# Performance work log

Hardware: AMD Instinct MI355X
Metric: run time of the kernel (lower is better)

The kernel has to match this reference:

```python
import jax, jax.numpy as jnp
import numpy as np

N_NODES = 50000
N_EDGES = 800000
IN_SIZE = 128
NUM_HEADS = 8
HEAD_DIM = IN_SIZE // NUM_HEADS  # qk/val head dim = 16


def setup_inputs() -> dict:
    key = jax.random.key(0)
    ks = jax.random.split(key, 16)
    d = IN_SIZE
    lim = 1.0 / np.sqrt(d)
    inp = {
        "in_feats": jax.random.normal(ks[0], (N_NODES, d), jnp.float32),
        "struc_feats": jax.random.normal(ks[1], (N_NODES, d), jnp.float32),
        "edge_weights": jax.random.uniform(ks[2], (N_EDGES,), jnp.float32),
        "ln_scale": jnp.ones((d,), jnp.float32),
        "ln_bias": jnp.zeros((d,), jnp.float32),
        "Ws": jax.random.uniform(ks[3], (d, d), jnp.float32, -lim, lim),
        "bs": jnp.zeros((d,), jnp.float32),
        "Wq": jax.random.uniform(ks[4], (d, d), jnp.float32, -lim, lim),
        "bq": jnp.zeros((d,), jnp.float32),
        "Wk": jax.random.uniform(ks[5], (d, d), jnp.float32, -lim, lim),
        "bk": jnp.zeros((d,), jnp.float32),
        "Wv": jax.random.uniform(ks[6], (d, d), jnp.float32, -lim, lim),
        "bv": jnp.zeros((d,), jnp.float32),
        "Wo": jax.random.uniform(ks[7], (d, d), jnp.float32, -lim, lim),
        "edge_ids": jax.random.randint(ks[8], (2, N_EDGES), 0, N_NODES, jnp.int64)
        if jax.config.jax_enable_x64 else jax.random.randint(ks[8], (2, N_EDGES), 0, N_NODES, jnp.int32),
    }
    return inp


def _layer_norm(x, scale, bias, eps=1e-5):
    mu = jnp.mean(x, axis=-1, keepdims=True)
    var = jnp.var(x, axis=-1, keepdims=True)
    return (x - mu) * jax.lax.rsqrt(var + eps) * scale + bias


def reference(in_feats, struc_feats, edge_weights, ln_scale, ln_bias,
              Ws, bs, Wq, bq, Wk, bk, Wv, bv, Wo, edge_ids):
    N = in_feats.shape[0]
    H, hd = NUM_HEADS, HEAD_DIM

    delta = _layer_norm(in_feats, ln_scale, ln_bias)           # pre-norm
    delta = jax.nn.gelu(delta, approximate=False)               # pre-activation (exact GELU, torch default)
    delta_struc = delta + struc_feats @ Ws.T + bs               # struc_proj add

    qry = (delta_struc @ Wq.T + bq) / np.sqrt(hd)                # [N, qk]
    keyf = delta_struc @ Wk.T + bk                               # [N, qk]
    val = delta @ Wv.T + bv                                      # [N, val]

    src, dst = edge_ids[0], edge_ids[1]                          # out[src] += A[src,dst] * val[dst]
    qe = qry[src].reshape(-1, H, hd)                             # [E, H, hd]
    ke = keyf[dst].reshape(-1, H, hd)                            # [E, H, hd]
    attn = jax.nn.sigmoid(jnp.sum(qe * ke, axis=-1))             # [E, H]
    attn = edge_weights[:, None] * attn

    msgs = attn[:, :, None] * val[dst].reshape(-1, H, hd)        # [E, H, hd]
    agg = jax.ops.segment_sum(msgs.reshape(-1, H * hd), src, num_segments=N)  # [N, val]

    out = agg @ Wo.T                                             # out_proj (no bias)
    return in_feats + out                                        # skip connection
```

## Files before the change

### kernel.cpp

```cpp
#include <hip/hip_runtime.h>
#include <math.h>

#define NF 128

typedef __attribute__((ext_vector_type(8))) short short8;
typedef __attribute__((ext_vector_type(4))) float floatx4;

__device__ __forceinline__ unsigned short f2bf(float f) {
    union { float x; unsigned int i; } c; c.x = f;
    unsigned int r = c.i + 0x7fffu + ((c.i >> 16) & 1u);
    return (unsigned short)(r >> 16);
}
__device__ __forceinline__ float bf2f(unsigned short u) {
    union { unsigned int i; float x; } c; c.i = ((unsigned int)u) << 16;
    return c.x;
}
__device__ __forceinline__ void unpack8(uint4 u, float* f) {
    union { unsigned int i; float x; } c;
    c.i = u.x << 16;          f[0] = c.x;
    c.i = u.x & 0xffff0000u;  f[1] = c.x;
    c.i = u.y << 16;          f[2] = c.x;
    c.i = u.y & 0xffff0000u;  f[3] = c.x;
    c.i = u.z << 16;          f[4] = c.x;
    c.i = u.z & 0xffff0000u;  f[5] = c.x;
    c.i = u.w << 16;          f[6] = c.x;
    c.i = u.w & 0xffff0000u;  f[7] = c.x;
}
__device__ __forceinline__ ushort4 pack4(float a, float b, float c, float d) {
    ushort4 h; h.x = f2bf(a); h.y = f2bf(b); h.z = f2bf(c); h.w = f2bf(d);
    return h;
}

__global__ __launch_bounds__(256) void wconv5_kernel(
    const float* __restrict__ a, const float* __restrict__ b,
    const float* __restrict__ c, const float* __restrict__ d,
    const float* __restrict__ e, unsigned short* __restrict__ o)
{
    int i = blockIdx.x * 256 + threadIdx.x;
    int w = i >> 14, j = i & 16383;
    const float* p = (w == 0) ? a : (w == 1) ? b : (w == 2) ? c : (w == 3) ? d : e;
    o[i] = f2bf(p[j]);
}


__device__ __forceinline__ void stage_w64(unsigned short (*Wh)[136],
                                          const unsigned short* Wg, int tid)
{
    const uint4* g = (const uint4*)Wg;
    #pragma unroll
    for (int p = 0; p < 4; ++p) {
        int idx = tid + p * 256;
        *(uint4*)&Wh[idx >> 4][(idx & 15) * 8] = g[idx];
    }
}

__device__ __forceinline__ void mfma4(const unsigned short (*A)[136],
                                      const unsigned short (*Wh)[136],
                                      int lg, int quad, int w, floatx4* acc4)
{
    #pragma unroll
    for (int ks = 0; ks < 4; ++ks) {
        short8 a = *(const short8*)&A[w * 16 + lg][ks * 32 + quad * 8];
        #pragma unroll
        for (int t = 0; t < 4; ++t) {
            short8 b = *(const short8*)&Wh[t * 16 + lg][ks * 32 + quad * 8];
            acc4[t] = __builtin_amdgcn_mfma_f32_16x16x32_bf16(a, b, acc4[t], 0, 0, 0);
        }
    }
}

__device__ __forceinline__ void emit_bf16(unsigned short (*Wst)[136],
                                          const floatx4* acc, const float* bias,
                                          float scale, unsigned short* outg,
                                          int m0, int M, int tid)
{
    int lane = tid & 63, w = tid >> 6, lg = lane & 15, quad = lane >> 4;
    __syncthreads();
    #pragma unroll
    for (int t = 0; t < 8; ++t) {
        int col = t * 16 + lg;
        float bvv = bias[col] * scale;
        #pragma unroll
        for (int r = 0; r < 4; ++r)
            Wst[w * 16 + quad * 4 + r][col] = f2bf(acc[t][r] * scale + bvv);
    }
    __syncthreads();
    #pragma unroll
    for (int p = 0; p < 4; ++p) {
        int idx = tid + p * 256;
        int row = idx >> 4, c16 = idx & 15;
        int gm = m0 + row;
        if (gm < M)
            *(uint4*)(outg + (size_t)gm * NF + c16 * 8) = *(const uint4*)&Wst[row][c16 * 8];
    }
    __syncthreads();
}

__global__ __launch_bounds__(256) void fused_node_kernel(
    const float* __restrict__ in_feats, const float* __restrict__ struc,
    const float* __restrict__ gamma, const float* __restrict__ beta,
    const unsigned short* __restrict__ Wall,
    const float* __restrict__ bs, const float* __restrict__ bq,
    const float* __restrict__ bk, const float* __restrict__ bv,
    unsigned short* __restrict__ qb, unsigned short* __restrict__ kb,
    unsigned short* __restrict__ vb, int M)
{
    __shared__ unsigned short Xd[64][136];
    __shared__ unsigned short Xs2[64][136];
    __shared__ unsigned short Wl[64][136];

    int tid = threadIdx.x;
    int m0 = blockIdx.x * 64;
    int lane = tid & 63, w = tid >> 6, lg = lane & 15, quad = lane >> 4;

    stage_w64(Wl, Wall, tid);
    {
        int row = tid >> 2, t4 = tid & 3;
        int gm = m0 + row;
        bool vr = gm < M;
        const float4* ip = (const float4*)(in_feats + (size_t)gm * NF) + t4 * 8;
        float4 xf[8];
        #pragma unroll
        for (int p = 0; p < 8; ++p)
            xf[p] = vr ? ip[p] : make_float4(0.f, 0.f, 0.f, 0.f);
        float s = 0.f, sq = 0.f;
        #pragma unroll
        for (int p = 0; p < 8; ++p) {
            s  += xf[p].x + xf[p].y + xf[p].z + xf[p].w;
            sq += xf[p].x * xf[p].x + xf[p].y * xf[p].y
                + xf[p].z * xf[p].z + xf[p].w * xf[p].w;
        }
        s  += __shfl_xor(s, 1, 64);  s  += __shfl_xor(s, 2, 64);
        sq += __shfl_xor(sq, 1, 64); sq += __shfl_xor(sq, 2, 64);
        float mu = s * (1.0f / 128.0f);
        float var = sq * (1.0f / 128.0f) - mu * mu;
        float rstd = rsqrtf(var + 1e-5f);
        const float4* gp = (const float4*)gamma + t4 * 8;
        const float4* bp = (const float4*)beta + t4 * 8;
        #pragma unroll
        for (int p = 0; p < 8; ++p) {
            float4 g4 = gp[p], b4 = bp[p];
            float o0 = (xf[p].x - mu) * rstd * g4.x + b4.x;
            float o1 = (xf[p].y - mu) * rstd * g4.y + b4.y;
            float o2 = (xf[p].z - mu) * rstd * g4.z + b4.z;
            float o3 = (xf[p].w - mu) * rstd * g4.w + b4.w;
            o0 = 0.5f * o0 * (1.0f + erff(o0 * 0.70710678118654752f));
            o1 = 0.5f * o1 * (1.0f + erff(o1 * 0.70710678118654752f));
            o2 = 0.5f * o2 * (1.0f + erff(o2 * 0.70710678118654752f));
            o3 = 0.5f * o3 * (1.0f + erff(o3 * 0.70710678118654752f));
            *(ushort4*)&Xd[row][t4 * 32 + p * 4] = pack4(o0, o1, o2, o3);
        }
        const float4* sp = (const float4*)(struc + (size_t)gm * NF) + t4 * 8;
        #pragma unroll
        for (int p = 0; p < 8; ++p) {
            float4 f = vr ? sp[p] : make_float4(0.f, 0.f, 0.f, 0.f);
            *(ushort4*)&Xs2[row][t4 * 32 + p * 4] = pack4(f.x, f.y, f.z, f.w);
        }
    }
    __syncthreads();

    floatx4 acc[8];
    #pragma unroll
    for (int t = 0; t < 8; ++t) acc[t] = (floatx4){0.f, 0.f, 0.f, 0.f};

    mfma4(Xs2, Wl, lg, quad, w, acc);
    __syncthreads();
    stage_w64(Wl, Wall + 8192, tid);
    __syncthreads();
    mfma4(Xs2, Wl, lg, quad, w, acc + 4);
    __syncthreads();

    #pragma unroll
    for (int t = 0; t < 8; ++t) {
        int col = t * 16 + lg;
        float bvv = bs[col];
        #pragma unroll
        for (int r = 0; r < 4; ++r) {
            int rl = w * 16 + quad * 4 + r;
            Xs2[rl][col] = f2bf(acc[t][r] + bvv + bf2f(Xd[rl][col]));
        }
    }
    stage_w64(Wl, Wall + 16384, tid);
    __syncthreads();

    #pragma unroll
    for (int t = 0; t < 8; ++t) acc[t] = (floatx4){0.f, 0.f, 0.f, 0.f};
    mfma4(Xs2, Wl, lg, quad, w, acc);
    __syncthreads();
    stage_w64(Wl, Wall + 16384 + 8192, tid);
    __syncthreads();
    mfma4(Xs2, Wl, lg, quad, w, acc + 4);
    emit_bf16(Wl, acc, bq, 0.25f, qb, m0, M, tid);

    stage_w64(Wl, Wall + 2 * 16384, tid);
    __syncthreads();
    #pragma unroll
    for (int t = 0; t < 8; ++t) acc[t] = (floatx4){0.f, 0.f, 0.f, 0.f};
    mfma4(Xs2, Wl, lg, quad, w, acc);
    __syncthreads();
    stage_w64(Wl, Wall + 2 * 16384 + 8192, tid);
    __syncthreads();
    mfma4(Xs2, Wl, lg, quad, w, acc + 4);
    emit_bf16(Wl, acc, bk, 1.0f, kb, m0, M, tid);

    stage_w64(Wl, Wall + 3 * 16384, tid);
    __syncthreads();
    #pragma unroll
    for (int t = 0; t < 8; ++t) acc[t] = (floatx4){0.f, 0.f, 0.f, 0.f};
    mfma4(Xd, Wl, lg, quad, w, acc);
    __syncthreads();
    stage_w64(Wl, Wall + 3 * 16384 + 8192, tid);
    __syncthreads();
    mfma4(Xd, Wl, lg, quad, w, acc + 4);
    emit_bf16(Wl, acc, bv, 1.0f, vb, m0, M, tid);
}

__global__ __launch_bounds__(256) void gemm_out_kernel(
    const unsigned short* __restrict__ Xb, const unsigned short* __restrict__ Wb,
    const float* __restrict__ addf, float* __restrict__ Y, int M)
{
    __shared__ unsigned short Xs[64][136];
    __shared__ unsigned short Wl[128][136];
    int tid = threadIdx.x;
    int m0 = blockIdx.x * 64;

    {
        const uint4* Wg = (const uint4*)Wb;
        #pragma unroll
        for (int p = 0; p < 8; ++p) {
            int idx = tid + p * 256;
            *(uint4*)&Wl[idx >> 4][(idx & 15) * 8] = Wg[idx];
        }
    }
    {
        const uint4* X = (const uint4*)Xb;
        #pragma unroll
        for (int p = 0; p < 4; ++p) {
            int idx = tid + p * 256;
            int row = idx >> 4, c16 = idx & 15;
            int gm = m0 + row;
            uint4 u = make_uint4(0u, 0u, 0u, 0u);
            if (gm < M) u = X[(size_t)gm * 16 + c16];
            *(uint4*)&Xs[row][c16 * 8] = u;
        }
    }
    __syncthreads();

    int lane = tid & 63, w = tid >> 6, lg = lane & 15, quad = lane >> 4;
    floatx4 acc[8];
    #pragma unroll
    for (int t = 0; t < 8; ++t) acc[t] = (floatx4){0.f, 0.f, 0.f, 0.f};
    #pragma unroll
    for (int ks = 0; ks < 4; ++ks) {
        short8 a = *(const short8*)&Xs[w * 16 + lg][ks * 32 + quad * 8];
        #pragma unroll
        for (int t = 0; t < 8; ++t) {
            short8 b = *(const short8*)&Wl[t * 16 + lg][ks * 32 + quad * 8];
            acc[t] = __builtin_amdgcn_mfma_f32_16x16x32_bf16(a, b, acc[t], 0, 0, 0);
        }
    }
    #pragma unroll
    for (int t = 0; t < 8; ++t) {
        int col = t * 16 + lg;
        #pragma unroll
        for (int r = 0; r < 4; ++r) {
            int gm = m0 + w * 16 + quad * 4 + r;
            if (gm >= M) continue;
            size_t off = (size_t)gm * NF + col;
            Y[off] = acc[t][r] + addf[off];
        }
    }
}

__global__ void hist_kernel(const int* __restrict__ eid, int* __restrict__ cnt, int E)
{
    int i = blockIdx.x * blockDim.x + threadIdx.x;
    if (i < E) atomicAdd(&cnt[eid[i]], 1);
}

__global__ __launch_bounds__(256) void scan1_kernel(
    const int* __restrict__ cnt, int* __restrict__ bsum, int n)
{
    int base = blockIdx.x * 1024;
    int s = 0;
    #pragma unroll
    for (int p = 0; p < 4; ++p) {
        int i = base + (int)threadIdx.x + p * 256;
        if (i < n) s += cnt[i];
    }
    #pragma unroll
    for (int m = 1; m <= 32; m <<= 1) s += __shfl_xor(s, m, 64);
    __shared__ int ws_[4];
    int wid = threadIdx.x >> 6;
    if ((threadIdx.x & 63) == 0) ws_[wid] = s;
    __syncthreads();
    if (threadIdx.x == 0) bsum[blockIdx.x] = ws_[0] + ws_[1] + ws_[2] + ws_[3];
}

__global__ __launch_bounds__(64) void scan2_kernel(
    int* __restrict__ bsum, int* __restrict__ row_start, int nb, int n)
{
    int lane = threadIdx.x;
    int v = (lane < nb) ? bsum[lane] : 0;
    int s = v;
    #pragma unroll
    for (int off = 1; off < 64; off <<= 1) {
        int t = __shfl_up(s, off, 64);
        if (lane >= off) s += t;
    }
    if (lane < nb) bsum[lane] = s - v;
    if (lane == 63) row_start[n] = s;
}

__global__ __launch_bounds__(256) void scan3_kernel(
    const int* __restrict__ cnt, const int* __restrict__ bsum,
    int* __restrict__ row_start, int* __restrict__ cursor, int n)
{
    int base = blockIdx.x * 1024;
    int tid = threadIdx.x, lane = tid & 63, wid = tid >> 6;
    int v[4]; int s = 0;
    #pragma unroll
    for (int p = 0; p < 4; ++p) {
        int i = base + tid * 4 + p;
        v[p] = (i < n) ? cnt[i] : 0;
        s += v[p];
    }
    int ss = s;
    #pragma unroll
    for (int off = 1; off < 64; off <<= 1) {
        int t = __shfl_up(ss, off, 64);
        if (lane >= off) ss += t;
    }
    __shared__ int wsum[4];
    if (lane == 63) wsum[wid] = ss;
    __syncthreads();
    int woff = 0;
    for (int j = 0; j < wid; ++j) woff += wsum[j];
    int a = bsum[blockIdx.x] + woff + (ss - s);
    #pragma unroll
    for (int p = 0; p < 4; ++p) {
        int i = base + tid * 4 + p;
        if (i < n) { row_start[i] = a; cursor[i] = a; a += v[p]; }
    }
}

__global__ void scatter_kernel(const int* __restrict__ eid, const float* __restrict__ ew,
                               int* __restrict__ cursor, int2* __restrict__ edata, int E)
{
    int i = blockIdx.x * blockDim.x + threadIdx.x;
    if (i < E) {
        int src = eid[i];
        int dst = eid[E + i];
        int pos = atomicAdd(&cursor[src], 1);
        edata[pos] = make_int2(dst, __float_as_int(ew[i]));
    }
}

__global__ __launch_bounds__(64) void aggregate_kernel(
    const unsigned short* __restrict__ Q, const unsigned short* __restrict__ Kf,
    const unsigned short* __restrict__ V, const int* __restrict__ row_start,
    const int2* __restrict__ edata, unsigned short* __restrict__ agg, int N)
{
    int node = blockIdx.x;
    int lane = threadIdx.x;
    int sg = lane >> 4, lg = lane & 15;
    int rs = row_start[node], re = row_start[node + 1];

    float qv[8];
    unpack8(*(const uint4*)(Q + (size_t)node * NF + lg * 8), qv);
    float acc[8];
    #pragma unroll
    for (int j = 0; j < 8; ++j) acc[j] = 0.f;

    int e = rs + sg;
    int2 ed = (e < re) ? edata[e] : make_int2(0, 0);
    for (int e0 = rs; e0 < re; e0 += 4) {
        int dst = ed.x;
        float wgt = __int_as_float(ed.y);
        int en = e0 + 4 + sg;
        int2 nxt = (en < re) ? edata[en] : make_int2(0, 0);

        float kv[8];
        unpack8(*(const uint4*)(Kf + (size_t)dst * NF + lg * 8), kv);
        float s = qv[0] * kv[0];
        #pragma unroll
        for (int j = 1; j < 8; ++j) s = fmaf(qv[j], kv[j], s);
        s += __shfl_xor(s, 1, 64);
        float a = wgt / (1.f + __expf(-s));

        float vv[8];
        unpack8(*(const uint4*)(V + (size_t)dst * NF + lg * 8), vv);
        #pragma unroll
        for (int j = 0; j < 8; ++j) acc[j] = fmaf(a, vv[j], acc[j]);
        ed = nxt;
    }
    #pragma unroll
    for (int j = 0; j < 8; ++j) {
        acc[j] += __shfl_xor(acc[j], 16, 64);
        acc[j] += __shfl_xor(acc[j], 32, 64);
    }
    if (sg == 0) {
        unsigned short* o = agg + (size_t)node * NF + lg * 8;
        *(ushort4*)o       = pack4(acc[0], acc[1], acc[2], acc[3]);
        *(ushort4*)(o + 4) = pack4(acc[4], acc[5], acc[6], acc[7]);
    }
}

extern "C" void kernel_launch(void* const* d_in, const int* in_sizes, int n_in,
                              void* d_out, int out_size, void* d_ws, size_t ws_size,
                              hipStream_t stream)
{
    const float* in_feats = (const float*)d_in[0];
    const float* struc    = (const float*)d_in[1];
    const float* eweights = (const float*)d_in[2];
    const float* ln_scale = (const float*)d_in[3];
    const float* ln_bias  = (const float*)d_in[4];
    const float* Ws       = (const float*)d_in[5];
    const float* bs       = (const float*)d_in[6];
    const float* Wq       = (const float*)d_in[7];
    const float* bq       = (const float*)d_in[8];
    const float* Wk       = (const float*)d_in[9];
    const float* bk       = (const float*)d_in[10];
    const float* Wv       = (const float*)d_in[11];
    const float* bv       = (const float*)d_in[12];
    const float* Wo       = (const float*)d_in[13];
    const int*   edge_ids = (const int*)d_in[14];
    float* out = (float*)d_out;

    int N = in_sizes[0] / NF;
    int E = in_sizes[2];

    size_t F = (size_t)N * NF;
    unsigned short* qb   = (unsigned short*)d_ws;
    unsigned short* kb   = qb + F;
    unsigned short* vb   = kb + F;
    unsigned short* aggb = vb + F;
    unsigned short* Wall = aggb + F;
    int2*  edata     = (int2*)(Wall + 5 * 16384);
    int*   cnt       = (int*)(edata + E);
    int*   row_start = cnt + N;
    int*   cursor    = row_start + N + 1;
    int*   bsum      = cursor + N;

    int gb  = (N + 63) / 64;
    int geb = (E + 255) / 256;
    int nb  = (N + 1023) / 1024;

    wconv5_kernel<<<(5 * 16384) / 256, 256, 0, stream>>>(Ws, Wq, Wk, Wv, Wo, Wall);

    hipMemsetAsync(cnt, 0, (size_t)N * sizeof(int), stream);
    hist_kernel<<<geb, 256, 0, stream>>>(edge_ids, cnt, E);
    scan1_kernel<<<nb, 256, 0, stream>>>(cnt, bsum, N);
    scan2_kernel<<<1, 64, 0, stream>>>(bsum, row_start, nb, N);
    scan3_kernel<<<nb, 256, 0, stream>>>(cnt, bsum, row_start, cursor, N);
    scatter_kernel<<<geb, 256, 0, stream>>>(edge_ids, eweights, cursor, edata, E);

    fused_node_kernel<<<gb, 256, 0, stream>>>(in_feats, struc, ln_scale, ln_bias,
                                              Wall, bs, bq, bk, bv, qb, kb, vb, N);

    aggregate_kernel<<<N, 64, 0, stream>>>(qb, kb, vb, row_start, edata, aggb, N);

    gemm_out_kernel<<<gb, 256, 0, stream>>>(aggb, Wall + 4 * 16384, in_feats, out, N);
}
```

Measured before the change: 328.5 us.

## Split fused node kernel, merge scan passes, batch aggregate nodes and unroll edges

The fused node kernel is split in two. One kernel computes delta and delta_struc and writes both to bf16 buffers, and a second kernel runs a 3-way grid over Q, K and V, each block holding the full weight in LDS. This trades extra global round-trips for more parallelism and fewer barriers. The scan2 kernel is removed: each scan3 block now sums the block totals itself. The aggregate kernel packs 4 nodes per 256-thread block and processes two edges per iteration to raise memory-level parallelism.

```diff
diff --git a/kernel.cpp b/kernel.cpp
--- a/kernel.cpp
+++ b/kernel.cpp
@@ -42,68 +42,11 @@
     o[i] = f2bf(p[j]);
 }
 
-
-__device__ __forceinline__ void stage_w64(unsigned short (*Wh)[136],
-                                          const unsigned short* Wg, int tid)
-{
-    const uint4* g = (const uint4*)Wg;
-    #pragma unroll
-    for (int p = 0; p < 4; ++p) {
-        int idx = tid + p * 256;
-        *(uint4*)&Wh[idx >> 4][(idx & 15) * 8] = g[idx];
-    }
-}
-
-__device__ __forceinline__ void mfma4(const unsigned short (*A)[136],
-                                      const unsigned short (*Wh)[136],
-                                      int lg, int quad, int w, floatx4* acc4)
-{
-    #pragma unroll
-    for (int ks = 0; ks < 4; ++ks) {
-        short8 a = *(const short8*)&A[w * 16 + lg][ks * 32 + quad * 8];
-        #pragma unroll
-        for (int t = 0; t < 4; ++t) {
-            short8 b = *(const short8*)&Wh[t * 16 + lg][ks * 32 + quad * 8];
-            acc4[t] = __builtin_amdgcn_mfma_f32_16x16x32_bf16(a, b, acc4[t], 0, 0, 0);
-        }
-    }
-}
-
-__device__ __forceinline__ void emit_bf16(unsigned short (*Wst)[136],
-                                          const floatx4* acc, const float* bias,
-                                          float scale, unsigned short* outg,
-                                          int m0, int M, int tid)
-{
-    int lane = tid & 63, w = tid >> 6, lg = lane & 15, quad = lane >> 4;
-    __syncthreads();
-    #pragma unroll
-    for (int t = 0; t < 8; ++t) {
-        int col = t * 16 + lg;
-        float bvv = bias[col] * scale;
-        #pragma unroll
-        for (int r = 0; r < 4; ++r)
-            Wst[w * 16 + quad * 4 + r][col] = f2bf(acc[t][r] * scale + bvv);
-    }
-    __syncthreads();
-    #pragma unroll
-    for (int p = 0; p < 4; ++p) {
-        int idx = tid + p * 256;
-        int row = idx >> 4, c16 = idx & 15;
-        int gm = m0 + row;
-        if (gm < M)
-            *(uint4*)(outg + (size_t)gm * NF + c16 * 8) = *(const uint4*)&Wst[row][c16 * 8];
-    }
-    __syncthreads();
-}
-
-__global__ __launch_bounds__(256) void fused_node_kernel(
+__global__ __launch_bounds__(256) void node_a_kernel(
     const float* __restrict__ in_feats, const float* __restrict__ struc,
     const float* __restrict__ gamma, const float* __restrict__ beta,
-    const unsigned short* __restrict__ Wall,
-    const float* __restrict__ bs, const float* __restrict__ bq,
-    const float* __restrict__ bk, const float* __restrict__ bv,
-    unsigned short* __restrict__ qb, unsigned short* __restrict__ kb,
-    unsigned short* __restrict__ vb, int M)
+    const unsigned short* __restrict__ Wsb, const float* __restrict__ bs,
+    unsigned short* __restrict__ deltab, unsigned short* __restrict__ dstrb, int M)
 {
     __shared__ unsigned short Xd[64][136];
     __shared__ unsigned short Xs2[64][136];
@@ -113,7 +56,14 @@
     int m0 = blockIdx.x * 64;
     int lane = tid & 63, w = tid >> 6, lg = lane & 15, quad = lane >> 4;
 
-    stage_w64(Wl, Wall, tid);
+    {
+        const uint4* g = (const uint4*)Wsb;
+        #pragma unroll
+        for (int p = 0; p < 4; ++p) {
+            int idx = tid + p * 256;
+            *(uint4*)&Wl[idx >> 4][(idx & 15) * 8] = g[idx];
+        }
+    }
     {
         int row = tid >> 2, t4 = tid & 3;
         int gm = m0 + row;
@@ -163,12 +113,34 @@
     #pragma unroll
     for (int t = 0; t < 8; ++t) acc[t] = (floatx4){0.f, 0.f, 0.f, 0.f};
 
-    mfma4(Xs2, Wl, lg, quad, w, acc);
-    __syncthreads();
-    stage_w64(Wl, Wall + 8192, tid);
-    __syncthreads();
-    mfma4(Xs2, Wl, lg, quad, w, acc + 4);
-    __syncthreads();
+    #pragma unroll
+    for (int ks = 0; ks < 4; ++ks) {
+        short8 a = *(const short8*)&Xs2[w * 16 + lg][ks * 32 + quad * 8];
+        #pragma unroll
+        for (int t = 0; t < 4; ++t) {
+            short8 b = *(const short8*)&Wl[t * 16 + lg][ks * 32 + quad * 8];
+            acc[t] = __builtin_amdgcn_mfma_f32_16x16x32_bf16(a, b, acc[t], 0, 0, 0);
+        }
+    }
+    __syncthreads();
+    {
+        const uint4* g = (const uint4*)(Wsb + 8192);
+        #pragma unroll
+        for (int p = 0; p < 4; ++p) {
+            int idx = tid + p * 256;
+            *(uint4*)&Wl[idx >> 4][(idx & 15) * 8] = g[idx];
+        }
+    }
+    __syncthreads();
+    #pragma unroll
+    for (int ks = 0; ks < 4; ++ks) {
+        short8 a = *(const short8*)&Xs2[w * 16 + lg][ks * 32 + quad * 8];
+        #pragma unroll
+        for (int t = 0; t < 4; ++t) {
+            short8 b = *(const short8*)&Wl[t * 16 + lg][ks * 32 + quad * 8];
+            acc[4 + t] = __builtin_amdgcn_mfma_f32_16x16x32_bf16(a, b, acc[4 + t], 0, 0, 0);
+        }
+    }
 
     #pragma unroll
     for (int t = 0; t < 8; ++t) {
@@ -180,39 +152,90 @@
             Xs2[rl][col] = f2bf(acc[t][r] + bvv + bf2f(Xd[rl][col]));
         }
     }
-    stage_w64(Wl, Wall + 16384, tid);
-    __syncthreads();
-
+    #pragma unroll
+    for (int p = 0; p < 4; ++p) {
+        int idx = lane + p * 64;
+        int row = w * 16 + (idx >> 4), c16 = idx & 15;
+        int gm = m0 + row;
+        if (gm < M) {
+            *(uint4*)(deltab + (size_t)gm * NF + c16 * 8) = *(const uint4*)&Xd[row][c16 * 8];
+            *(uint4*)(dstrb  + (size_t)gm * NF + c16 * 8) = *(const uint4*)&Xs2[row][c16 * 8];
+        }
+    }
+}
+
+__global__ __launch_bounds__(256) void node_qkv_kernel(
+    const unsigned short* __restrict__ deltab, const unsigned short* __restrict__ dstrb,
+    const unsigned short* __restrict__ Wall, const float* __restrict__ bq,
+    const float* __restrict__ bk, const float* __restrict__ bv,
+    unsigned short* __restrict__ qb, unsigned short* __restrict__ kb,
+    unsigned short* __restrict__ vb, int M)
+{
+    __shared__ unsigned short Xs[64][136];
+    __shared__ unsigned short Wl[128][136];
+
+    int tid = threadIdx.x;
+    int m0 = blockIdx.x * 64;
+    int y = blockIdx.y;
+    int lane = tid & 63, w = tid >> 6, lg = lane & 15, quad = lane >> 4;
+
+    const unsigned short* Xg = (y == 2) ? deltab : dstrb;
+    const unsigned short* Wg = Wall + (y + 1) * 16384;
+    const float* bias = (y == 0) ? bq : (y == 1) ? bk : bv;
+    float scale = (y == 0) ? 0.25f : 1.0f;
+    unsigned short* outg = (y == 0) ? qb : (y == 1) ? kb : vb;
+
+    {
+        const uint4* g = (const uint4*)Wg;
+        #pragma unroll
+        for (int p = 0; p < 8; ++p) {
+            int idx = tid + p * 256;
+            *(uint4*)&Wl[idx >> 4][(idx & 15) * 8] = g[idx];
+        }
+    }
+    {
+        const uint4* X = (const uint4*)Xg;
+        #pragma unroll
+        for (int p = 0; p < 4; ++p) {
+            int idx = lane + p * 64;
+            int row = w * 16 + (idx >> 4), c16 = idx & 15;
+            int gm = m0 + row;
+            uint4 u = make_uint4(0u, 0u, 0u, 0u);
+            if (gm < M) u = X[(size_t)gm * 16 + c16];
+            *(uint4*)&Xs[row][c16 * 8] = u;
+        }
+    }
+    __syncthreads();
+
+    floatx4 acc[8];
     #pragma unroll
     for (int t = 0; t < 8; ++t) acc[t] = (floatx4){0.f, 0.f, 0.f, 0.f};
-    mfma4(Xs2, Wl, lg, quad, w, acc);
-    __syncthreads();
-    stage_w64(Wl, Wall + 16384 + 8192, tid);
-    __syncthreads();
-    mfma4(Xs2, Wl, lg, quad, w, acc + 4);
-    emit_bf16(Wl, acc, bq, 0.25f, qb, m0, M, tid);
-
-    stage_w64(Wl, Wall + 2 * 16384, tid);
-    __syncthreads();
-    #pragma unroll
-    for (int t = 0; t < 8; ++t) acc[t] = (floatx4){0.f, 0.f, 0.f, 0.f};
-    mfma4(Xs2, Wl, lg, quad, w, acc);
-    __syncthreads();
-    stage_w64(Wl, Wall + 2 * 16384 + 8192, tid);
-    __syncthreads();
-    mfma4(Xs2, Wl, lg, quad, w, acc + 4);
-    emit_bf16(Wl, acc, bk, 1.0f, kb, m0, M, tid);
-
-    stage_w64(Wl, Wall + 3 * 16384, tid);
-    __syncthreads();
-    #pragma unroll
-    for (int t = 0; t < 8; ++t) acc[t] = (floatx4){0.f, 0.f, 0.f, 0.f};
-    mfma4(Xd, Wl, lg, quad, w, acc);
-    __syncthreads();
-    stage_w64(Wl, Wall + 3 * 16384 + 8192, tid);
-    __syncthreads();
-    mfma4(Xd, Wl, lg, quad, w, acc + 4);
-    emit_bf16(Wl, acc, bv, 1.0f, vb, m0, M, tid);
+    #pragma unroll
+    for (int ks = 0; ks < 4; ++ks) {
+        short8 a = *(const short8*)&Xs[w * 16 + lg][ks * 32 + quad * 8];
+        #pragma unroll
+        for (int t = 0; t < 8; ++t) {
+            short8 b = *(const short8*)&Wl[t * 16 + lg][ks * 32 + quad * 8];
+            acc[t] = __builtin_amdgcn_mfma_f32_16x16x32_bf16(a, b, acc[t], 0, 0, 0);
+        }
+    }
+
+    #pragma unroll
+    for (int t = 0; t < 8; ++t) {
+        int col = t * 16 + lg;
+        float bvv = bias[col];
+        #pragma unroll
+        for (int r = 0; r < 4; ++r)
+            Xs[w * 16 + quad * 4 + r][col] = f2bf((acc[t][r] + bvv) * scale);
+    }
+    #pragma unroll
+    for (int p = 0; p < 4; ++p) {
+        int idx = lane + p * 64;
+        int row = w * 16 + (idx >> 4), c16 = idx & 15;
+        int gm = m0 + row;
+        if (gm < M)
+            *(uint4*)(outg + (size_t)gm * NF + c16 * 8) = *(const uint4*)&Xs[row][c16 * 8];
+    }
 }
 
 __global__ __launch_bounds__(256) void gemm_out_kernel(
@@ -223,21 +246,22 @@
     __shared__ unsigned short Wl[128][136];
     int tid = threadIdx.x;
     int m0 = blockIdx.x * 64;
-
-    {
-        const uint4* Wg = (const uint4*)Wb;
+    int lane = tid & 63, w = tid >> 6, lg = lane & 15, quad = lane >> 4;
+
+    {
+        const uint4* g = (const uint4*)Wb;
         #pragma unroll
         for (int p = 0; p < 8; ++p) {
             int idx = tid + p * 256;
-            *(uint4*)&Wl[idx >> 4][(idx & 15) * 8] = Wg[idx];
+            *(uint4*)&Wl[idx >> 4][(idx & 15) * 8] = g[idx];
         }
     }
     {
         const uint4* X = (const uint4*)Xb;
         #pragma unroll
         for (int p = 0; p < 4; ++p) {
-            int idx = tid + p * 256;
-            int row = idx >> 4, c16 = idx & 15;
+            int idx = lane + p * 64;
+            int row = w * 16 + (idx >> 4), c16 = idx & 15;
             int gm = m0 + row;
             uint4 u = make_uint4(0u, 0u, 0u, 0u);
             if (gm < M) u = X[(size_t)gm * 16 + c16];
@@ -246,7 +270,6 @@
     }
     __syncthreads();
 
-    int lane = tid & 63, w = tid >> 6, lg = lane & 15, quad = lane >> 4;
     floatx4 acc[8];
     #pragma unroll
     for (int t = 0; t < 8; ++t) acc[t] = (floatx4){0.f, 0.f, 0.f, 0.f};
@@ -297,27 +320,23 @@
     if (threadIdx.x == 0) bsum[blockIdx.x] = ws_[0] + ws_[1] + ws_[2] + ws_[3];
 }
 
-__global__ __launch_bounds__(64) void scan2_kernel(
-    int* __restrict__ bsum, int* __restrict__ row_start, int nb, int n)
-{
-    int lane = threadIdx.x;
-    int v = (lane < nb) ? bsum[lane] : 0;
-    int s = v;
-    #pragma unroll
-    for (int off = 1; off < 64; off <<= 1) {
-        int t = __shfl_up(s, off, 64);
-        if (lane >= off) s += t;
-    }
-    if (lane < nb) bsum[lane] = s - v;
-    if (lane == 63) row_start[n] = s;
-}
-
 __global__ __launch_bounds__(256) void scan3_kernel(
     const int* __restrict__ cnt, const int* __restrict__ bsum,
-    int* __restrict__ row_start, int* __restrict__ cursor, int n)
-{
+    int* __restrict__ row_start, int* __restrict__ cursor, int n, int nb)
+{
+    __shared__ int base_off;
+    int tid = threadIdx.x, lane = tid & 63, wid = tid >> 6;
+    if (tid == 0) {
+        int a = 0;
+        for (int j = 0; j < (int)blockIdx.x; ++j) a += bsum[j];
+        base_off = a;
+        if ((int)blockIdx.x == nb - 1) {
+            int tot = a;
+            for (int j = blockIdx.x; j < nb; ++j) tot += bsum[j];
+            row_start[n] = tot;
+        }
+    }
     int base = blockIdx.x * 1024;
-    int tid = threadIdx.x, lane = tid & 63, wid = tid >> 6;
     int v[4]; int s = 0;
     #pragma unroll
     for (int p = 0; p < 4; ++p) {
@@ -336,7 +355,7 @@
     __syncthreads();
     int woff = 0;
     for (int j = 0; j < wid; ++j) woff += wsum[j];
-    int a = bsum[blockIdx.x] + woff + (ss - s);
+    int a = base_off + woff + (ss - s);
     #pragma unroll
     for (int p = 0; p < 4; ++p) {
         int i = base + tid * 4 + p;
@@ -356,13 +375,14 @@
     }
 }
 
-__global__ __launch_bounds__(64) void aggregate_kernel(
+__global__ __launch_bounds__(256) void aggregate_kernel(
     const unsigned short* __restrict__ Q, const unsigned short* __restrict__ Kf,
     const unsigned short* __restrict__ V, const int* __restrict__ row_start,
     const int2* __restrict__ edata, unsigned short* __restrict__ agg, int N)
 {
-    int node = blockIdx.x;
-    int lane = threadIdx.x;
+    int node = blockIdx.x * 4 + (threadIdx.x >> 6);
+    if (node >= N) return;
+    int lane = threadIdx.x & 63;
     int sg = lane >> 4, lg = lane & 15;
     int rs = row_start[node], re = row_start[node + 1];
 
@@ -372,27 +392,38 @@
     #pragma unroll
     for (int j = 0; j < 8; ++j) acc[j] = 0.f;
 
-    int e = rs + sg;
-    int2 ed = (e < re) ? edata[e] : make_int2(0, 0);
-    for (int e0 = rs; e0 < re; e0 += 4) {
-        int dst = ed.x;
-        float wgt = __int_as_float(ed.y);
-        int en = e0 + 4 + sg;
-        int2 nxt = (en < re) ? edata[en] : make_int2(0, 0);
-
-        float kv[8];
-        unpack8(*(const uint4*)(Kf + (size_t)dst * NF + lg * 8), kv);
-        float s = qv[0] * kv[0];
-        #pragma unroll
-        for (int j = 1; j < 8; ++j) s = fmaf(qv[j], kv[j], s);
-        s += __shfl_xor(s, 1, 64);
-        float a = wgt / (1.f + __expf(-s));
-
-        float vv[8];
-        unpack8(*(const uint4*)(V + (size_t)dst * NF + lg * 8), vv);
-        #pragma unroll
-        for (int j = 0; j < 8; ++j) acc[j] = fmaf(a, vv[j], acc[j]);
-        ed = nxt;
+    int e1 = rs + sg, e2 = rs + sg + 4;
+    int2 ed1 = (e1 < re) ? edata[e1] : make_int2(0, 0);
+    int2 ed2 = (e2 < re) ? edata[e2] : make_int2(0, 0);
+
+    for (int e0 = rs; e0 < re; e0 += 8) {
+        int2 c1 = ed1, c2 = ed2;
+        int en1 = e0 + 8 + sg, en2 = en1 + 4;
+        ed1 = (en1 < re) ? edata[en1] : make_int2(0, 0);
+        ed2 = (en2 < re) ? edata[en2] : make_int2(0, 0);
+
+        float kv1[8], kv2[8];
+        unpack8(*(const uint4*)(Kf + (size_t)c1.x * NF + lg * 8), kv1);
+        unpack8(*(const uint4*)(Kf + (size_t)c2.x * NF + lg * 8), kv2);
+        float s1 = qv[0] * kv1[0], s2 = qv[0] * kv2[0];
+        #pragma unroll
+        for (int j = 1; j < 8; ++j) {
+            s1 = fmaf(qv[j], kv1[j], s1);
+            s2 = fmaf(qv[j], kv2[j], s2);
+        }
+        s1 += __shfl_xor(s1, 1, 64);
+        s2 += __shfl_xor(s2, 1, 64);
+        float a1 = __int_as_float(c1.y) / (1.f + __expf(-s1));
+        float a2 = __int_as_float(c2.y) / (1.f + __expf(-s2));
+
+        float vv1[8], vv2[8];
+        unpack8(*(const uint4*)(V + (size_t)c1.x * NF + lg * 8), vv1);
+        unpack8(*(const uint4*)(V + (size_t)c2.x * NF + lg * 8), vv2);
+        #pragma unroll
+        for (int j = 0; j < 8; ++j) {
+            acc[j] = fmaf(a1, vv1[j], acc[j]);
+            acc[j] = fmaf(a2, vv2[j], acc[j]);
+        }
     }
     #pragma unroll
     for (int j = 0; j < 8; ++j) {
@@ -431,11 +462,13 @@
     int E = in_sizes[2];
 
     size_t F = (size_t)N * NF;
-    unsigned short* qb   = (unsigned short*)d_ws;
-    unsigned short* kb   = qb + F;
-    unsigned short* vb   = kb + F;
-    unsigned short* aggb = vb + F;
-    unsigned short* Wall = aggb + F;
+    unsigned short* deltab = (unsigned short*)d_ws;
+    unsigned short* dstrb  = deltab + F;
+    unsigned short* qb     = dstrb + F;
+    unsigned short* kb     = qb + F;
+    unsigned short* vb     = kb + F;
+    unsigned short* aggb   = vb + F;
+    unsigned short* Wall   = aggb + F;
     int2*  edata     = (int2*)(Wall + 5 * 16384);
     int*   cnt       = (int*)(edata + E);
     int*   row_start = cnt + N;
@@ -451,14 +484,15 @@
     hipMemsetAsync(cnt, 0, (size_t)N * sizeof(int), stream);
     hist_kernel<<<geb, 256, 0, stream>>>(edge_ids, cnt, E);
     scan1_kernel<<<nb, 256, 0, stream>>>(cnt, bsum, N);
-    scan2_kernel<<<1, 64, 0, stream>>>(bsum, row_start, nb, N);
-    scan3_kernel<<<nb, 256, 0, stream>>>(cnt, bsum, row_start, cursor, N);
+    scan3_kernel<<<nb, 256, 0, stream>>>(cnt, bsum, row_start, cursor, N, nb);
     scatter_kernel<<<geb, 256, 0, stream>>>(edge_ids, eweights, cursor, edata, E);
 
-    fused_node_kernel<<<gb, 256, 0, stream>>>(in_feats, struc, ln_scale, ln_bias,
-                                              Wall, bs, bq, bk, bv, qb, kb, vb, N);
-
-    aggregate_kernel<<<N, 64, 0, stream>>>(qb, kb, vb, row_start, edata, aggb, N);
+    node_a_kernel<<<gb, 256, 0, stream>>>(in_feats, struc, ln_scale, ln_bias,
+                                          Wall, bs, deltab, dstrb, N);
+    node_qkv_kernel<<<dim3(gb, 3), 256, 0, stream>>>(deltab, dstrb, Wall,
+                                                     bq, bk, bv, qb, kb, vb, N);
+
+    aggregate_kernel<<<(N + 3) / 4, 256, 0, stream>>>(qb, kb, vb, row_start, edata, aggb, N);
 
     gemm_out_kernel<<<gb, 256, 0, stream>>>(aggb, Wall + 4 * 16384, in_feats, out, N);
 }
```

Result: slower. 337.5 us (+2.7%).
